# Performance work log

Hardware: AMD Instinct MI355X
Metric: run time of the kernel (lower is better)

The kernel has to match this reference:

```python
import jax, jax.numpy as jnp
import numpy as np

N_NODES = 100000
N_EDGES = 3200000
D_IN = 128
D_HID = 128
D_FF = 256
N_CLASSES = 26
N_GRAPHS = 512


def setup_inputs() -> dict:
    key = jax.random.key(0)
    ks = jax.random.split(key, 12)
    s = 0.05
    return {
        "x": jax.random.normal(ks[0], (N_NODES, D_IN), dtype=jnp.float32),
        "edge_index": jax.random.randint(ks[1], (2, N_EDGES), 0, N_NODES, dtype=jnp.int64),
        "batch": jnp.sort(jax.random.randint(ks[2], (N_NODES,), 0, N_GRAPHS, dtype=jnp.int64)),
        "W1": jax.random.normal(ks[3], (D_IN, D_HID), dtype=jnp.float32) * s,
        "b1": jnp.zeros((D_HID,), dtype=jnp.float32),
        "W2": jax.random.normal(ks[4], (D_HID, D_HID), dtype=jnp.float32) * s,
        "b2": jnp.zeros((D_HID,), dtype=jnp.float32),
        "W3": jax.random.normal(ks[5], (D_HID, D_HID), dtype=jnp.float32) * s,
        "b3": jnp.zeros((D_HID,), dtype=jnp.float32),
        "Wfc": jax.random.normal(ks[6], (D_HID, D_FF), dtype=jnp.float32) * s,
        "bfc": jnp.zeros((D_FF,), dtype=jnp.float32),
        "Wfc2": jax.random.normal(ks[7], (D_FF, N_CLASSES), dtype=jnp.float32) * s,
        "bfc2": jnp.zeros((N_CLASSES,), dtype=jnp.float32),
    }


def _gcn_layer(x, src, dst, norm, W, b):
    # GCNConv: h = x @ W; out[dst] += norm_e * h[src]; out += b
    h = x @ W                                   # [N, D]
    msg = h[src] * norm[:, None]                # [E+N, D] gather + scale
    agg = jax.ops.segment_sum(msg, dst, num_segments=N_NODES)
    return agg + b


def reference(x, edge_index, batch, W1, b1, W2, b2, W3, b3, Wfc, bfc, Wfc2, bfc2):
    # add self-loops (PyG GCNConv default) and compute symmetric normalization once
    loop = jnp.arange(N_NODES, dtype=edge_index.dtype)
    src = jnp.concatenate([edge_index[0], loop])
    dst = jnp.concatenate([edge_index[1], loop])
    deg = jax.ops.segment_sum(jnp.ones_like(dst, dtype=x.dtype), dst, num_segments=N_NODES)
    dinv = jnp.where(deg > 0, jax.lax.rsqrt(deg), 0.0)
    norm = dinv[src] * dinv[dst]               # D^{-1/2} A_hat D^{-1/2}

    h = jax.nn.relu(_gcn_layer(x, src, dst, norm, W1, b1))
    h = jax.nn.relu(_gcn_layer(h, src, dst, norm, W2, b2))
    h = jax.nn.relu(_gcn_layer(h, src, dst, norm, W3, b3))

    # global mean pool over graphs
    sums = jax.ops.segment_sum(h, batch, num_segments=N_GRAPHS)       # [G, D]
    cnts = jax.ops.segment_sum(jnp.ones((h.shape[0],), h.dtype), batch, num_segments=N_GRAPHS)
    pooled = sums / jnp.maximum(cnts, 1.0)[:, None]

    out = jax.nn.relu(pooled @ Wfc + bfc)       # dropout is identity at inference
    return out @ Wfc2 + bfc2                    # [G, num_classes]
```

## Files before the change

### kernel.cpp

```cpp
#include <hip/hip_runtime.h>
#include <hip/hip_bf16.h>

typedef __bf16 bf16;
typedef __attribute__((ext_vector_type(8))) __bf16 bf16x8;
typedef __attribute__((ext_vector_type(4))) float f32x4;

constexpr int N_NODES   = 100000;
constexpr int N_PAD     = 100032;
constexpr int D         = 128;
constexpr int D_FF      = 256;
constexpr int N_CLASSES = 26;
constexpr int N_GRAPHS  = 512;
constexpr int NB1       = 256;
constexpr int NBUCK     = (N_NODES + 511) / 512;

__device__ inline float2 bf2f(unsigned u) {
    float lo = __uint_as_float(u << 16);
    float hi = __uint_as_float(u & 0xffff0000u);
    return make_float2(lo, hi);
}

__device__ inline void nt_store_bf16(bf16* p, float f) {
    bf16 v = (bf16)f;
    short s = *reinterpret_cast<short*>(&v);
    __builtin_nontemporal_store(s, reinterpret_cast<short*>(p));
}


__global__ __launch_bounds__(1024) void p1_hist(const int* __restrict__ edst,
                                                int* __restrict__ gcount, int e) {
    __shared__ int cnt[NBUCK];
    for (int t = threadIdx.x; t < NBUCK; t += 1024) cnt[t] = 0;
    __syncthreads();
    int chunk = (e + NB1 - 1) / NB1;
    int lo = blockIdx.x * chunk;
    int hi = min(e, lo + chunk);
    for (int i = lo + threadIdx.x; i < hi; i += 1024)
        atomicAdd(&cnt[edst[i] >> 9], 1);
    __syncthreads();
    for (int t = threadIdx.x; t < NBUCK; t += 1024)
        gcount[t * NB1 + blockIdx.x] = cnt[t];
}

__global__ __launch_bounds__(256) void scan1(const int* __restrict__ in,
                                             int* out, int* bsum, int n) {
    __shared__ int sd[256];
    int i = blockIdx.x * 256 + threadIdx.x;
    int v = (i < n) ? in[i] : 0;
    sd[threadIdx.x] = v; __syncthreads();
    for (int off = 1; off < 256; off <<= 1) {
        int t = (threadIdx.x >= off) ? sd[threadIdx.x - off] : 0;
        __syncthreads();
        sd[threadIdx.x] += t;
        __syncthreads();
    }
    if (i < n) out[i] = sd[threadIdx.x] - v;
    if (threadIdx.x == 255) bsum[blockIdx.x] = sd[255];
}

__global__ __launch_bounds__(1024) void misc_kernel(const int* __restrict__ bsum,
                                                    int* __restrict__ boff, int nb,
                                                    const int* __restrict__ batch,
                                                    int* __restrict__ starts, int n,
                                                    const float* __restrict__ W0,
                                                    const float* __restrict__ W1,
                                                    const float* __restrict__ W2,
                                                    bf16* __restrict__ WT3,
                                                    float* __restrict__ gsum) {
    int t = threadIdx.x;
    if (blockIdx.x == 0) {
        if (t <= N_GRAPHS) {
            int lo = 0, hi = n;
            while (lo < hi) {
                int mid = (lo + hi) >> 1;
                if (batch[mid] < t) lo = mid + 1; else hi = mid;
            }
            starts[t] = lo;
        }
        __shared__ int sd[1024];
        int v = (t < nb) ? bsum[t] : 0;
        sd[t] = v; __syncthreads();
        for (int off = 1; off < 1024; off <<= 1) {
            int x = (t >= off) ? sd[t - off] : 0;
            __syncthreads();
            sd[t] += x;
            __syncthreads();
        }
        if (t < nb) boff[t] = sd[t] - v;
    } else if (blockIdx.x <= 48) {
        int idx = (blockIdx.x - 1) * 1024 + t;
        int l = idx >> 14;
        int rem = idx & 16383;
        int nn = rem >> 7;
        int kk = rem & 127;
        const float* W = (l == 0) ? W0 : (l == 1) ? W1 : W2;
        WT3[idx] = (bf16)W[kk * D + nn];
    } else {
        int idx = (blockIdx.x - 49) * 1024 + t;
        f32x4 z = {0.f, 0.f, 0.f, 0.f};
        *((f32x4*)gsum + idx) = z;
    }
}

__global__ __launch_bounds__(1024) void p3_scatter(const int* __restrict__ esrc,
                                                   const int* __restrict__ edst,
                                                   const int* __restrict__ gbase,
                                                   const int* __restrict__ boff,
                                                   int* __restrict__ ebuf, int e) {
    __shared__ int cur[NBUCK];
    for (int t = threadIdx.x; t < NBUCK; t += 1024)
        cur[t] = gbase[t * NB1 + blockIdx.x] + boff[t];
    __syncthreads();
    int chunk = (e + NB1 - 1) / NB1;
    int lo = blockIdx.x * chunk;
    int hi = min(e, lo + chunk);
    for (int i = lo + threadIdx.x; i < hi; i += 1024) {
        int d = edst[i], s = esrc[i];
        int pos = atomicAdd(&cur[d >> 9], 1);
        ebuf[pos] = (s << 9) | (d & 511);
    }
}

__global__ __launch_bounds__(1024) void p45_fill(const int* __restrict__ ebuf,
                                                 const int* __restrict__ gbase,
                                                 const int* __restrict__ boff,
                                                 float* __restrict__ dinv,
                                                 int* __restrict__ rowptr,
                                                 int* __restrict__ csrc, int e, int n) {
    __shared__ int cnt[512];
    __shared__ int ps[512];
    __shared__ int cur[512];
    int b = blockIdx.x, t = threadIdx.x;
    if (t < 512) cnt[t] = 0;
    __syncthreads();
    int lo = gbase[b * NB1] + boff[b];
    int hi = (b + 1 < NBUCK) ? gbase[(b + 1) * NB1] + boff[b + 1] : e;
    for (int i = lo + t; i < hi; i += 1024)
        atomicAdd(&cnt[ebuf[i] & 511], 1);
    __syncthreads();
    int a = (t < 512) ? cnt[t] : 0;
    if (t < 512) ps[t] = a;
    __syncthreads();
    for (int off = 1; off < 512; off <<= 1) {
        int v = (t >= off && t < 512) ? ps[t - off] : 0;
        __syncthreads();
        if (t < 512) ps[t] += v;
        __syncthreads();
    }
    if (t < 512) {
        int g0 = lo + ps[t] - a;
        int node = b * 512 + t;
        cur[t] = g0;
        if (node < n) {
            rowptr[node] = g0;
            dinv[node] = 1.0f / sqrtf((float)(a + 1));
        }
    }
    if (b == 0 && t == 0) rowptr[n] = e;
    __syncthreads();
    for (int i = lo + t; i < hi; i += 1024) {
        int pe = ebuf[i];
        int pos = atomicAdd(&cur[pe & 511], 1);
        csrc[pos] = pe >> 9;
    }
}


__global__ __launch_bounds__(256) void gemm_f32_kernel(const float* __restrict__ A,
                                                       const bf16* __restrict__ WT,
                                                       bf16* __restrict__ C,
                                                       const float* __restrict__ dinv, int n) {
    int wave = threadIdx.x >> 6;
    int lane = threadIdx.x & 63;
    int m16  = lane & 15;
    int quad = lane >> 4;
    int row0 = blockIdx.x * 64 + wave * 16;
    int arowi = row0 + m16;

    bf16x8 a[4];
    const float* arow = A + (size_t)arowi * D + quad * 8;
#pragma unroll
    for (int kt = 0; kt < 4; ++kt) {
        f32x4 f0 = {0.f, 0.f, 0.f, 0.f};
        f32x4 f1 = {0.f, 0.f, 0.f, 0.f};
        if (arowi < n) {
            f0 = __builtin_nontemporal_load((const f32x4*)(arow + kt * 32));
            f1 = __builtin_nontemporal_load((const f32x4*)(arow + kt * 32 + 4));
        }
        bf16x8 v = { (bf16)f0[0], (bf16)f0[1], (bf16)f0[2], (bf16)f0[3],
                     (bf16)f1[0], (bf16)f1[1], (bf16)f1[2], (bf16)f1[3] };
        a[kt] = v;
    }

    float sc[4];
#pragma unroll
    for (int r = 0; r < 4; ++r) {
        int rr = row0 + quad * 4 + r;
        sc[r] = (rr < n) ? dinv[rr] : 0.f;
    }

#pragma unroll
    for (int nt = 0; nt < 8; ++nt) {
        f32x4 acc = {0.f, 0.f, 0.f, 0.f};
        const bf16* brow = WT + (nt * 16 + m16) * D + quad * 8;
#pragma unroll
        for (int kt = 0; kt < 4; ++kt) {
            bf16x8 b = *(const bf16x8*)(brow + kt * 32);
            acc = __builtin_amdgcn_mfma_f32_16x16x32_bf16(a[kt], b, acc, 0, 0, 0);
        }
#pragma unroll
        for (int r = 0; r < 4; ++r)
            nt_store_bf16(&C[(row0 + quad * 4 + r) * D + nt * 16 + m16], sc[r] * acc[r]);
    }
}

__device__ inline void agg_node(const bf16* __restrict__ h, int v, int n, int c,
                                const int* __restrict__ rowptr,
                                const int* __restrict__ csrc,
                                const float* __restrict__ dinv,
                                float& dv, float acc[8]) {
    int s = 0, e = 0;
    dv = 0.f;
    if (v < n) { s = rowptr[v]; e = rowptr[v + 1]; dv = dinv[v]; }
#pragma unroll
    for (int d = 0; d < 8; ++d) acc[d] = 0.f;
    if (v < n) {
        uint4 u = *(const uint4*)(h + (size_t)v * D + c * 8);
        float2 f0 = bf2f(u.x), f1 = bf2f(u.y), f2 = bf2f(u.z), f3 = bf2f(u.w);
        acc[0] = f0.x; acc[1] = f0.y; acc[2] = f1.x; acc[3] = f1.y;
        acc[4] = f2.x; acc[5] = f2.y; acc[6] = f3.x; acc[7] = f3.y;
    }
    int j = s;
    for (; j + 3 < e; j += 4) {
        int s0 = __builtin_nontemporal_load(csrc + j);
        int s1 = __builtin_nontemporal_load(csrc + j + 1);
        int s2 = __builtin_nontemporal_load(csrc + j + 2);
        int s3 = __builtin_nontemporal_load(csrc + j + 3);
        uint4 u0 = *(const uint4*)(h + (size_t)s0 * D + c * 8);
        uint4 u1 = *(const uint4*)(h + (size_t)s1 * D + c * 8);
        uint4 u2 = *(const uint4*)(h + (size_t)s2 * D + c * 8);
        uint4 u3 = *(const uint4*)(h + (size_t)s3 * D + c * 8);
        {
            float2 a0 = bf2f(u0.x), a1 = bf2f(u0.y), a2 = bf2f(u0.z), a3 = bf2f(u0.w);
            acc[0] += a0.x; acc[1] += a0.y; acc[2] += a1.x; acc[3] += a1.y;
            acc[4] += a2.x; acc[5] += a2.y; acc[6] += a3.x; acc[7] += a3.y;
        }
        {
            float2 a0 = bf2f(u1.x), a1 = bf2f(u1.y), a2 = bf2f(u1.z), a3 = bf2f(u1.w);
            acc[0] += a0.x; acc[1] += a0.y; acc[2] += a1.x; acc[3] += a1.y;
            acc[4] += a2.x; acc[5] += a2.y; acc[6] += a3.x; acc[7] += a3.y;
        }
        {
            float2 a0 = bf2f(u2.x), a1 = bf2f(u2.y), a2 = bf2f(u2.z), a3 = bf2f(u2.w);
            acc[0] += a0.x; acc[1] += a0.y; acc[2] += a1.x; acc[3] += a1.y;
            acc[4] += a2.x; acc[5] += a2.y; acc[6] += a3.x; acc[7] += a3.y;
        }
        {
            float2 a0 = bf2f(u3.x), a1 = bf2f(u3.y), a2 = bf2f(u3.z), a3 = bf2f(u3.w);
            acc[0] += a0.x; acc[1] += a0.y; acc[2] += a1.x; acc[3] += a1.y;
            acc[4] += a2.x; acc[5] += a2.y; acc[6] += a3.x; acc[7] += a3.y;
        }
    }
    for (; j < e; ++j) {
        int s0 = __builtin_nontemporal_load(csrc + j);
        uint4 u0 = *(const uint4*)(h + (size_t)s0 * D + c * 8);
        float2 a0 = bf2f(u0.x), a1 = bf2f(u0.y), a2 = bf2f(u0.z), a3 = bf2f(u0.w);
        acc[0] += a0.x; acc[1] += a0.y; acc[2] += a1.x; acc[3] += a1.y;
        acc[4] += a2.x; acc[5] += a2.y; acc[6] += a3.x; acc[7] += a3.y;
    }
}

__global__ __launch_bounds__(256) void spmm_gemm_kernel(const bf16* __restrict__ h,
                                                        const int* __restrict__ rowptr,
                                                        const int* __restrict__ csrc,
                                                        const float* __restrict__ dinv,
                                                        const float* __restrict__ bias,
                                                        const bf16* __restrict__ WT,
                                                        bf16* __restrict__ C, int n) {
    __shared__ bf16 tile[16][136];
    int t = threadIdx.x;
    int grp = t >> 4;
    int c   = t & 15;
    int v   = blockIdx.x * 16 + grp;
    float dv, acc[8];
    agg_node(h, v, n, c, rowptr, csrc, dinv, dv, acc);
    {
        float4 bi0 = *(const float4*)(bias + c * 8);
        float4 bi1 = *(const float4*)(bias + c * 8 + 4);
        bf16x8 o;
        o[0] = (bf16)fmaxf(fmaf(dv, acc[0], bi0.x), 0.f);
        o[1] = (bf16)fmaxf(fmaf(dv, acc[1], bi0.y), 0.f);
        o[2] = (bf16)fmaxf(fmaf(dv, acc[2], bi0.z), 0.f);
        o[3] = (bf16)fmaxf(fmaf(dv, acc[3], bi0.w), 0.f);
        o[4] = (bf16)fmaxf(fmaf(dv, acc[4], bi1.x), 0.f);
        o[5] = (bf16)fmaxf(fmaf(dv, acc[5], bi1.y), 0.f);
        o[6] = (bf16)fmaxf(fmaf(dv, acc[6], bi1.z), 0.f);
        o[7] = (bf16)fmaxf(fmaf(dv, acc[7], bi1.w), 0.f);
        *(bf16x8*)(&tile[grp][c * 8]) = o;
    }
    __syncthreads();

    int wave = t >> 6, lane = t & 63;
    int m16 = lane & 15, quad = lane >> 4;
    bf16x8 a[4];
#pragma unroll
    for (int kt = 0; kt < 4; ++kt)
        a[kt] = *(const bf16x8*)(&tile[m16][quad * 8 + kt * 32]);

    int base = blockIdx.x * 16;
    float sc[4];
#pragma unroll
    for (int r = 0; r < 4; ++r) {
        int rr = base + quad * 4 + r;
        sc[r] = (rr < n) ? dinv[rr] : 0.f;
    }

#pragma unroll
    for (int nt2 = 0; nt2 < 2; ++nt2) {
        int nt = wave * 2 + nt2;
        f32x4 accq = {0.f, 0.f, 0.f, 0.f};
        const bf16* brow = WT + (nt * 16 + m16) * D + quad * 8;
#pragma unroll
        for (int kt = 0; kt < 4; ++kt) {
            bf16x8 b = *(const bf16x8*)(brow + kt * 32);
            accq = __builtin_amdgcn_mfma_f32_16x16x32_bf16(a[kt], b, accq, 0, 0, 0);
        }
#pragma unroll
        for (int r = 0; r < 4; ++r)
            nt_store_bf16(&C[(size_t)(base + quad * 4 + r) * D + nt * 16 + m16],
                          sc[r] * accq[r]);
    }
}

__global__ __launch_bounds__(256) void spmm2_pool_kernel(const bf16* __restrict__ h,
                                                         const int* __restrict__ rowptr,
                                                         const int* __restrict__ csrc,
                                                         const float* __restrict__ dinv,
                                                         const float* __restrict__ bias,
                                                         const int* __restrict__ batch,
                                                         float* __restrict__ gsum, int n) {
    __shared__ float tile[16][D];
    __shared__ int gid[16];
    int t = threadIdx.x;
    int grp = t >> 4;
    int c   = t & 15;
    int v   = blockIdx.x * 16 + grp;
    float dv, acc[8];
    agg_node(h, v, n, c, rowptr, csrc, dinv, dv, acc);
    float4 bi0 = *(const float4*)(bias + c * 8);
    float4 bi1 = *(const float4*)(bias + c * 8 + 4);
    float r0 = fmaxf(fmaf(dv, acc[0], bi0.x), 0.f);
    float r1 = fmaxf(fmaf(dv, acc[1], bi0.y), 0.f);
    float r2 = fmaxf(fmaf(dv, acc[2], bi0.z), 0.f);
    float r3 = fmaxf(fmaf(dv, acc[3], bi0.w), 0.f);
    float r4 = fmaxf(fmaf(dv, acc[4], bi1.x), 0.f);
    float r5 = fmaxf(fmaf(dv, acc[5], bi1.y), 0.f);
    float r6 = fmaxf(fmaf(dv, acc[6], bi1.z), 0.f);
    float r7 = fmaxf(fmaf(dv, acc[7], bi1.w), 0.f);
    if (v >= n) { r0 = r1 = r2 = r3 = r4 = r5 = r6 = r7 = 0.f; }
    tile[grp][c * 8 + 0] = r0; tile[grp][c * 8 + 1] = r1;
    tile[grp][c * 8 + 2] = r2; tile[grp][c * 8 + 3] = r3;
    tile[grp][c * 8 + 4] = r4; tile[grp][c * 8 + 5] = r5;
    tile[grp][c * 8 + 6] = r6; tile[grp][c * 8 + 7] = r7;
    if (c == 0) gid[grp] = (v < n) ? batch[v] : -1;
    __syncthreads();
    if (t < D) {
        int curg = gid[0];
        float sum = 0.f;
        if (curg >= 0) {
#pragma unroll 1
            for (int k = 0; k < 16; ++k) {
                int gg = gid[k];
                if (gg < 0) break;
                if (gg != curg) {
                    atomicAdd(&gsum[(size_t)curg * D + t], sum);
                    curg = gg; sum = 0.f;
                }
                sum += tile[k][t];
            }
            atomicAdd(&gsum[(size_t)curg * D + t], sum);
        }
    }
}

__global__ __launch_bounds__(256) void fc_head_kernel(const float* __restrict__ gsum,
                                                      const int* __restrict__ starts,
                                                      const float* __restrict__ Wfc,
                                                      const float* __restrict__ bfc,
                                                      const float* __restrict__ Wfc2,
                                                      const float* __restrict__ bfc2,
                                                      float* __restrict__ out) {
    __shared__ float pr[D];
    __shared__ float hid[D_FF];
    __shared__ float red[N_CLASSES][9];
    int g = blockIdx.x, t = threadIdx.x;
    if (t < D) {
        float ccount = fmaxf((float)(starts[g + 1] - starts[g]), 1.0f);
        pr[t] = gsum[(size_t)g * D + t] / ccount;
    }
    __syncthreads();
    float a0 = 0.f, a1 = 0.f, a2 = 0.f, a3 = 0.f;
    for (int k = 0; k < D; k += 4) {
        a0 = fmaf(pr[k],     Wfc[k * D_FF + t],       a0);
        a1 = fmaf(pr[k + 1], Wfc[(k + 1) * D_FF + t], a1);
        a2 = fmaf(pr[k + 2], Wfc[(k + 2) * D_FF + t], a2);
        a3 = fmaf(pr[k + 3], Wfc[(k + 3) * D_FF + t], a3);
    }
    hid[t] = fmaxf((a0 + a1) + (a2 + a3) + bfc[t], 0.f);
    __syncthreads();
    if (t < N_CLASSES * 8) {
        int cls = t >> 3, kk = t & 7;
        float o = 0.f;
        for (int k = kk; k < D_FF; k += 8)
            o = fmaf(hid[k], Wfc2[k * N_CLASSES + cls], o);
        red[cls][kk] = o;
    }
    __syncthreads();
    if (t < N_CLASSES) {
        float o = bfc2[t];
#pragma unroll
        for (int k = 0; k < 8; ++k) o += red[t][k];
        out[g * N_CLASSES + t] = o;
    }
}


extern "C" void kernel_launch(void* const* d_in, const int* in_sizes, int n_in,
                              void* d_out, int out_size, void* d_ws, size_t ws_size,
                              hipStream_t stream) {
    const float* x     = (const float*)d_in[0];
    const int*   eidx  = (const int*)d_in[1];
    const int*   batch = (const int*)d_in[2];
    const float* W[3]  = { (const float*)d_in[3], (const float*)d_in[5], (const float*)d_in[7] };
    const float* b[3]  = { (const float*)d_in[4], (const float*)d_in[6], (const float*)d_in[8] };
    const float* Wfc   = (const float*)d_in[9];
    const float* bfc   = (const float*)d_in[10];
    const float* Wfc2  = (const float*)d_in[11];
    const float* bfc2  = (const float*)d_in[12];
    float* out = (float*)d_out;

    const int E = in_sizes[1] / 2;
    const int N = in_sizes[0] / D;
    const int* esrc = eidx;
    const int* edst = eidx + E;

    uint8_t* base = (uint8_t*)d_ws;
    size_t off = 0;
    auto alloc = [&](size_t bytes) -> void* {
        void* p = base + off;
        off = (off + bytes + 255) & ~(size_t)255;
        return p;
    };
    bf16*  hA     = (bf16*) alloc((size_t)N_PAD * D * 2);
    bf16*  hB     = (bf16*) alloc((size_t)N_PAD * D * 2);
    bf16*  WT3    = (bf16*) alloc((size_t)3 * D * D * 2);
    int*   csrc   = (int*)  alloc((size_t)E * 4);
    int*   ebuf   = (int*)  alloc((size_t)E * 4);
    int*   gcount = (int*)  alloc((size_t)NBUCK * NB1 * 4);
    int*   gbase  = (int*)  alloc((size_t)(NBUCK * NB1 + 1) * 4);
    int*   rowptr = (int*)  alloc((size_t)(N + 1) * 4);
    float* dinv   = (float*)alloc((size_t)N * 4);
    int*   bsum   = (int*)  alloc(4096);
    int*   boff   = (int*)  alloc(4096);
    int*   starts = (int*)  alloc((size_t)(N_GRAPHS + 1) * 4);
    float* gsum   = (float*)alloc((size_t)N_GRAPHS * D * 4);
    (void)ws_size; (void)n_in; (void)out_size;

    const int GB  = N_PAD / 64;
    const int SGB = (N + 15) / 16;
    const int GCN = NBUCK * NB1;
    const int GCB = (GCN + 255) / 256;

    p1_hist<<<NB1, 1024, 0, stream>>>(edst, gcount, E);
    scan1<<<GCB, 256, 0, stream>>>(gcount, gbase, bsum, GCN);
    misc_kernel<<<65, 1024, 0, stream>>>(bsum, boff, GCB, batch, starts, N,
                                         W[0], W[1], W[2], WT3, gsum);
    p3_scatter<<<NB1, 1024, 0, stream>>>(esrc, edst, gbase, boff, ebuf, E);
    p45_fill<<<NBUCK, 1024, 0, stream>>>(ebuf, gbase, boff, dinv, rowptr, csrc, E, N);

    gemm_f32_kernel<<<GB, 256, 0, stream>>>(x, WT3, hA, dinv, N);
    spmm_gemm_kernel<<<SGB, 256, 0, stream>>>(hA, rowptr, csrc, dinv, b[0],
                                              WT3 + (size_t)1 * D * D, hB, N);
    spmm_gemm_kernel<<<SGB, 256, 0, stream>>>(hB, rowptr, csrc, dinv, b[1],
                                              WT3 + (size_t)2 * D * D, hA, N);
    spmm2_pool_kernel<<<SGB, 256, 0, stream>>>(hA, rowptr, csrc, dinv, b[2],
                                               batch, gsum, N);

    fc_head_kernel<<<N_GRAPHS, 256, 0, stream>>>(gsum, starts, Wfc, bfc, Wfc2, bfc2, out);
}
```

Measured before the change: 617.6 us.

## Fuse GCN layers and head into one cooperative persistent kernel with grid syncs

Replaces the separate GEMM, two SpMM+GEMM, SpMM+pool and FC-head launches with one cooperative persistent kernel that grid-strides over tiles and uses grid.sync between stages. The histogram and misc setup kernels are merged into one launch, and the block scan gets its own small kernel. Nontemporal loads and stores are also replaced with plain accesses. The aim is to cut launch overhead and inter-kernel gaps, at the cost of grid-wide barriers, persistent-loop overhead and occupancy limited to co-resident blocks.

After: 1.279 ms. +107.0%, slower.

```diff
diff --git a/kernel.cpp b/kernel.cpp
--- a/kernel.cpp
+++ b/kernel.cpp
@@ -1,5 +1,8 @@
 #include <hip/hip_runtime.h>
 #include <hip/hip_bf16.h>
+#include <hip/hip_cooperative_groups.h>
+
+namespace cg = cooperative_groups;
 
 typedef __bf16 bf16;
 typedef __attribute__((ext_vector_type(8))) __bf16 bf16x8;
@@ -13,6 +16,8 @@
 constexpr int N_GRAPHS  = 512;
 constexpr int NB1       = 256;
 constexpr int NBUCK     = (N_NODES + 511) / 512;
+constexpr int GB        = N_PAD / 64;
+constexpr int SGB       = N_NODES / 16;
 
 __device__ inline float2 bf2f(unsigned u) {
     float lo = __uint_as_float(u << 16);
@@ -20,26 +25,54 @@
     return make_float2(lo, hi);
 }
 
-__device__ inline void nt_store_bf16(bf16* p, float f) {
-    bf16 v = (bf16)f;
-    short s = *reinterpret_cast<short*>(&v);
-    __builtin_nontemporal_store(s, reinterpret_cast<short*>(p));
-}
-
-
-__global__ __launch_bounds__(1024) void p1_hist(const int* __restrict__ edst,
-                                                int* __restrict__ gcount, int e) {
-    __shared__ int cnt[NBUCK];
-    for (int t = threadIdx.x; t < NBUCK; t += 1024) cnt[t] = 0;
-    __syncthreads();
-    int chunk = (e + NB1 - 1) / NB1;
-    int lo = blockIdx.x * chunk;
-    int hi = min(e, lo + chunk);
-    for (int i = lo + threadIdx.x; i < hi; i += 1024)
-        atomicAdd(&cnt[edst[i] >> 9], 1);
-    __syncthreads();
-    for (int t = threadIdx.x; t < NBUCK; t += 1024)
-        gcount[t * NB1 + blockIdx.x] = cnt[t];
+
+__global__ __launch_bounds__(1024) void p1misc_kernel(const int* __restrict__ edst,
+                                                      int* __restrict__ gcount, int e,
+                                                      const int* __restrict__ batch,
+                                                      int* __restrict__ starts, int n,
+                                                      const float* __restrict__ W0,
+                                                      const float* __restrict__ W1,
+                                                      const float* __restrict__ W2,
+                                                      bf16* __restrict__ WT3,
+                                                      float* __restrict__ gsum) {
+    int t = threadIdx.x;
+    if (blockIdx.x < NB1) {
+        __shared__ int cnt[NBUCK];
+        for (int q = t; q < NBUCK; q += 1024) cnt[q] = 0;
+        __syncthreads();
+        int chunk = (e + NB1 - 1) / NB1;
+        int lo = blockIdx.x * chunk;
+        int hi = min(e, lo + chunk);
+        for (int i = lo + t; i < hi; i += 1024)
+            atomicAdd(&cnt[edst[i] >> 9], 1);
+        __syncthreads();
+        for (int q = t; q < NBUCK; q += 1024)
+            gcount[q * NB1 + blockIdx.x] = cnt[q];
+    } else {
+        int mb = blockIdx.x - NB1;
+        if (mb == 0) {
+            if (t <= N_GRAPHS) {
+                int lo = 0, hi = n;
+                while (lo < hi) {
+                    int mid = (lo + hi) >> 1;
+                    if (batch[mid] < t) lo = mid + 1; else hi = mid;
+                }
+                starts[t] = lo;
+            }
+        } else if (mb <= 48) {
+            int idx = (mb - 1) * 1024 + t;
+            int l = idx >> 14;
+            int rem = idx & 16383;
+            int nn = rem >> 7;
+            int kk = rem & 127;
+            const float* W = (l == 0) ? W0 : (l == 1) ? W1 : W2;
+            WT3[idx] = (bf16)W[kk * D + nn];
+        } else {
+            int idx = (mb - 49) * 1024 + t;
+            f32x4 z = {0.f, 0.f, 0.f, 0.f};
+            *((f32x4*)gsum + idx) = z;
+        }
+    }
 }
 
 __global__ __launch_bounds__(256) void scan1(const int* __restrict__ in,
@@ -58,48 +91,19 @@
     if (threadIdx.x == 255) bsum[blockIdx.x] = sd[255];
 }
 
-__global__ __launch_bounds__(1024) void misc_kernel(const int* __restrict__ bsum,
-                                                    int* __restrict__ boff, int nb,
-                                                    const int* __restrict__ batch,
-                                                    int* __restrict__ starts, int n,
-                                                    const float* __restrict__ W0,
-                                                    const float* __restrict__ W1,
-                                                    const float* __restrict__ W2,
-                                                    bf16* __restrict__ WT3,
-                                                    float* __restrict__ gsum) {
+__global__ __launch_bounds__(1024) void scan2k(const int* __restrict__ bsum,
+                                               int* __restrict__ boff, int nb) {
+    __shared__ int sd[1024];
     int t = threadIdx.x;
-    if (blockIdx.x == 0) {
-        if (t <= N_GRAPHS) {
-            int lo = 0, hi = n;
-            while (lo < hi) {
-                int mid = (lo + hi) >> 1;
-                if (batch[mid] < t) lo = mid + 1; else hi = mid;
-            }
-            starts[t] = lo;
-        }
-        __shared__ int sd[1024];
-        int v = (t < nb) ? bsum[t] : 0;
-        sd[t] = v; __syncthreads();
-        for (int off = 1; off < 1024; off <<= 1) {
-            int x = (t >= off) ? sd[t - off] : 0;
-            __syncthreads();
-            sd[t] += x;
-            __syncthreads();
-        }
-        if (t < nb) boff[t] = sd[t] - v;
-    } else if (blockIdx.x <= 48) {
-        int idx = (blockIdx.x - 1) * 1024 + t;
-        int l = idx >> 14;
-        int rem = idx & 16383;
-        int nn = rem >> 7;
-        int kk = rem & 127;
-        const float* W = (l == 0) ? W0 : (l == 1) ? W1 : W2;
-        WT3[idx] = (bf16)W[kk * D + nn];
-    } else {
-        int idx = (blockIdx.x - 49) * 1024 + t;
-        f32x4 z = {0.f, 0.f, 0.f, 0.f};
-        *((f32x4*)gsum + idx) = z;
-    }
+    int v = (t < nb) ? bsum[t] : 0;
+    sd[t] = v; __syncthreads();
+    for (int off = 1; off < 1024; off <<= 1) {
+        int x = (t >= off) ? sd[t - off] : 0;
+        __syncthreads();
+        sd[t] += x;
+        __syncthreads();
+    }
+    if (t < nb) boff[t] = sd[t] - v;
 }
 
 __global__ __launch_bounds__(1024) void p3_scatter(const int* __restrict__ esrc,
@@ -165,55 +169,6 @@
     }
 }
 
-
-__global__ __launch_bounds__(256) void gemm_f32_kernel(const float* __restrict__ A,
-                                                       const bf16* __restrict__ WT,
-                                                       bf16* __restrict__ C,
-                                                       const float* __restrict__ dinv, int n) {
-    int wave = threadIdx.x >> 6;
-    int lane = threadIdx.x & 63;
-    int m16  = lane & 15;
-    int quad = lane >> 4;
-    int row0 = blockIdx.x * 64 + wave * 16;
-    int arowi = row0 + m16;
-
-    bf16x8 a[4];
-    const float* arow = A + (size_t)arowi * D + quad * 8;
-#pragma unroll
-    for (int kt = 0; kt < 4; ++kt) {
-        f32x4 f0 = {0.f, 0.f, 0.f, 0.f};
-        f32x4 f1 = {0.f, 0.f, 0.f, 0.f};
-        if (arowi < n) {
-            f0 = __builtin_nontemporal_load((const f32x4*)(arow + kt * 32));
-            f1 = __builtin_nontemporal_load((const f32x4*)(arow + kt * 32 + 4));
-        }
-        bf16x8 v = { (bf16)f0[0], (bf16)f0[1], (bf16)f0[2], (bf16)f0[3],
-                     (bf16)f1[0], (bf16)f1[1], (bf16)f1[2], (bf16)f1[3] };
-        a[kt] = v;
-    }
-
-    float sc[4];
-#pragma unroll
-    for (int r = 0; r < 4; ++r) {
-        int rr = row0 + quad * 4 + r;
-        sc[r] = (rr < n) ? dinv[rr] : 0.f;
-    }
-
-#pragma unroll
-    for (int nt = 0; nt < 8; ++nt) {
-        f32x4 acc = {0.f, 0.f, 0.f, 0.f};
-        const bf16* brow = WT + (nt * 16 + m16) * D + quad * 8;
-#pragma unroll
-        for (int kt = 0; kt < 4; ++kt) {
-            bf16x8 b = *(const bf16x8*)(brow + kt * 32);
-            acc = __builtin_amdgcn_mfma_f32_16x16x32_bf16(a[kt], b, acc, 0, 0, 0);
-        }
-#pragma unroll
-        for (int r = 0; r < 4; ++r)
-            nt_store_bf16(&C[(row0 + quad * 4 + r) * D + nt * 16 + m16], sc[r] * acc[r]);
-    }
-}
-
 __device__ inline void agg_node(const bf16* __restrict__ h, int v, int n, int c,
                                 const int* __restrict__ rowptr,
                                 const int* __restrict__ csrc,
@@ -232,10 +187,7 @@
     }
     int j = s;
     for (; j + 3 < e; j += 4) {
-        int s0 = __builtin_nontemporal_load(csrc + j);
-        int s1 = __builtin_nontemporal_load(csrc + j + 1);
-        int s2 = __builtin_nontemporal_load(csrc + j + 2);
-        int s3 = __builtin_nontemporal_load(csrc + j + 3);
+        int s0 = csrc[j], s1 = csrc[j + 1], s2 = csrc[j + 2], s3 = csrc[j + 3];
         uint4 u0 = *(const uint4*)(h + (size_t)s0 * D + c * 8);
         uint4 u1 = *(const uint4*)(h + (size_t)s1 * D + c * 8);
         uint4 u2 = *(const uint4*)(h + (size_t)s2 * D + c * 8);
@@ -262,7 +214,7 @@
         }
     }
     for (; j < e; ++j) {
-        int s0 = __builtin_nontemporal_load(csrc + j);
+        int s0 = csrc[j];
         uint4 u0 = *(const uint4*)(h + (size_t)s0 * D + c * 8);
         float2 a0 = bf2f(u0.x), a1 = bf2f(u0.y), a2 = bf2f(u0.z), a3 = bf2f(u0.w);
         acc[0] += a0.x; acc[1] += a0.y; acc[2] += a1.x; acc[3] += a1.y;
@@ -270,23 +222,24 @@
     }
 }
 
-__global__ __launch_bounds__(256) void spmm_gemm_kernel(const bf16* __restrict__ h,
-                                                        const int* __restrict__ rowptr,
-                                                        const int* __restrict__ csrc,
-                                                        const float* __restrict__ dinv,
-                                                        const float* __restrict__ bias,
-                                                        const bf16* __restrict__ WT,
-                                                        bf16* __restrict__ C, int n) {
-    __shared__ bf16 tile[16][136];
+__device__ inline void agg_gemm_tiles(const bf16* __restrict__ h,
+                                      const int* __restrict__ rowptr,
+                                      const int* __restrict__ csrc,
+                                      const float* __restrict__ dinv,
+                                      const float* __restrict__ bias,
+                                      const bf16* __restrict__ WT,
+                                      bf16* __restrict__ C, int n,
+                                      bf16 (*tb)[136]) {
     int t = threadIdx.x;
-    int grp = t >> 4;
-    int c   = t & 15;
-    int v   = blockIdx.x * 16 + grp;
-    float dv, acc[8];
-    agg_node(h, v, n, c, rowptr, csrc, dinv, dv, acc);
-    {
-        float4 bi0 = *(const float4*)(bias + c * 8);
-        float4 bi1 = *(const float4*)(bias + c * 8 + 4);
+    int grp = t >> 4, c = t & 15;
+    int wave = t >> 6, lane = t & 63;
+    int m16 = lane & 15, quad = lane >> 4;
+    float4 bi0 = *(const float4*)(bias + c * 8);
+    float4 bi1 = *(const float4*)(bias + c * 8 + 4);
+    for (int tile = blockIdx.x; tile < SGB; tile += gridDim.x) {
+        int v = tile * 16 + grp;
+        float dv, acc[8];
+        agg_node(h, v, n, c, rowptr, csrc, dinv, dv, acc);
         bf16x8 o;
         o[0] = (bf16)fmaxf(fmaf(dv, acc[0], bi0.x), 0.f);
         o[1] = (bf16)fmaxf(fmaf(dv, acc[1], bi0.y), 0.f);
@@ -296,131 +249,179 @@
         o[5] = (bf16)fmaxf(fmaf(dv, acc[5], bi1.y), 0.f);
         o[6] = (bf16)fmaxf(fmaf(dv, acc[6], bi1.z), 0.f);
         o[7] = (bf16)fmaxf(fmaf(dv, acc[7], bi1.w), 0.f);
-        *(bf16x8*)(&tile[grp][c * 8]) = o;
-    }
-    __syncthreads();
-
-    int wave = t >> 6, lane = t & 63;
-    int m16 = lane & 15, quad = lane >> 4;
-    bf16x8 a[4];
-#pragma unroll
-    for (int kt = 0; kt < 4; ++kt)
-        a[kt] = *(const bf16x8*)(&tile[m16][quad * 8 + kt * 32]);
-
-    int base = blockIdx.x * 16;
-    float sc[4];
-#pragma unroll
-    for (int r = 0; r < 4; ++r) {
-        int rr = base + quad * 4 + r;
-        sc[r] = (rr < n) ? dinv[rr] : 0.f;
-    }
-
-#pragma unroll
-    for (int nt2 = 0; nt2 < 2; ++nt2) {
-        int nt = wave * 2 + nt2;
-        f32x4 accq = {0.f, 0.f, 0.f, 0.f};
-        const bf16* brow = WT + (nt * 16 + m16) * D + quad * 8;
-#pragma unroll
-        for (int kt = 0; kt < 4; ++kt) {
-            bf16x8 b = *(const bf16x8*)(brow + kt * 32);
-            accq = __builtin_amdgcn_mfma_f32_16x16x32_bf16(a[kt], b, accq, 0, 0, 0);
-        }
-#pragma unroll
-        for (int r = 0; r < 4; ++r)
-            nt_store_bf16(&C[(size_t)(base + quad * 4 + r) * D + nt * 16 + m16],
-                          sc[r] * accq[r]);
-    }
-}
-
-__global__ __launch_bounds__(256) void spmm2_pool_kernel(const bf16* __restrict__ h,
-                                                         const int* __restrict__ rowptr,
-                                                         const int* __restrict__ csrc,
-                                                         const float* __restrict__ dinv,
-                                                         const float* __restrict__ bias,
-                                                         const int* __restrict__ batch,
-                                                         float* __restrict__ gsum, int n) {
-    __shared__ float tile[16][D];
-    __shared__ int gid[16];
-    int t = threadIdx.x;
-    int grp = t >> 4;
-    int c   = t & 15;
-    int v   = blockIdx.x * 16 + grp;
-    float dv, acc[8];
-    agg_node(h, v, n, c, rowptr, csrc, dinv, dv, acc);
-    float4 bi0 = *(const float4*)(bias + c * 8);
-    float4 bi1 = *(const float4*)(bias + c * 8 + 4);
-    float r0 = fmaxf(fmaf(dv, acc[0], bi0.x), 0.f);
-    float r1 = fmaxf(fmaf(dv, acc[1], bi0.y), 0.f);
-    float r2 = fmaxf(fmaf(dv, acc[2], bi0.z), 0.f);
-    float r3 = fmaxf(fmaf(dv, acc[3], bi0.w), 0.f);
-    float r4 = fmaxf(fmaf(dv, acc[4], bi1.x), 0.f);
-    float r5 = fmaxf(fmaf(dv, acc[5], bi1.y), 0.f);
-    float r6 = fmaxf(fmaf(dv, acc[6], bi1.z), 0.f);
-    float r7 = fmaxf(fmaf(dv, acc[7], bi1.w), 0.f);
-    if (v >= n) { r0 = r1 = r2 = r3 = r4 = r5 = r6 = r7 = 0.f; }
-    tile[grp][c * 8 + 0] = r0; tile[grp][c * 8 + 1] = r1;
-    tile[grp][c * 8 + 2] = r2; tile[grp][c * 8 + 3] = r3;
-    tile[grp][c * 8 + 4] = r4; tile[grp][c * 8 + 5] = r5;
-    tile[grp][c * 8 + 6] = r6; tile[grp][c * 8 + 7] = r7;
-    if (c == 0) gid[grp] = (v < n) ? batch[v] : -1;
-    __syncthreads();
-    if (t < D) {
-        int curg = gid[0];
-        float sum = 0.f;
-        if (curg >= 0) {
-#pragma unroll 1
-            for (int k = 0; k < 16; ++k) {
-                int gg = gid[k];
-                if (gg < 0) break;
-                if (gg != curg) {
-                    atomicAdd(&gsum[(size_t)curg * D + t], sum);
-                    curg = gg; sum = 0.f;
-                }
-                sum += tile[k][t];
+        __syncthreads();
+        *(bf16x8*)(&tb[grp][c * 8]) = o;
+        __syncthreads();
+
+        bf16x8 a[4];
+#pragma unroll
+        for (int kt = 0; kt < 4; ++kt)
+            a[kt] = *(const bf16x8*)(&tb[m16][quad * 8 + kt * 32]);
+        int base = tile * 16;
+        float sc[4];
+#pragma unroll
+        for (int r = 0; r < 4; ++r) {
+            int rr = base + quad * 4 + r;
+            sc[r] = (rr < n) ? dinv[rr] : 0.f;
+        }
+#pragma unroll
+        for (int nt2 = 0; nt2 < 2; ++nt2) {
+            int nt = wave * 2 + nt2;
+            f32x4 q = {0.f, 0.f, 0.f, 0.f};
+            const bf16* brow = WT + (nt * 16 + m16) * D + quad * 8;
+#pragma unroll
+            for (int kt = 0; kt < 4; ++kt) {
+                bf16x8 bfr = *(const bf16x8*)(brow + kt * 32);
+                q = __builtin_amdgcn_mfma_f32_16x16x32_bf16(a[kt], bfr, q, 0, 0, 0);
             }
-            atomicAdd(&gsum[(size_t)curg * D + t], sum);
-        }
-    }
-}
-
-__global__ __launch_bounds__(256) void fc_head_kernel(const float* __restrict__ gsum,
-                                                      const int* __restrict__ starts,
-                                                      const float* __restrict__ Wfc,
-                                                      const float* __restrict__ bfc,
-                                                      const float* __restrict__ Wfc2,
-                                                      const float* __restrict__ bfc2,
-                                                      float* __restrict__ out) {
+#pragma unroll
+            for (int r = 0; r < 4; ++r)
+                C[(size_t)(base + quad * 4 + r) * D + nt * 16 + m16] = (bf16)(sc[r] * q[r]);
+        }
+    }
+}
+
+__global__ __launch_bounds__(256, 8) void mega_kernel(
+        const float* __restrict__ x, const bf16* __restrict__ WT3,
+        bf16* __restrict__ hA, bf16* __restrict__ hB,
+        const int* __restrict__ rowptr, const int* __restrict__ csrc,
+        const float* __restrict__ dinv,
+        const float* __restrict__ b0, const float* __restrict__ b1,
+        const float* __restrict__ b2,
+        const int* __restrict__ batch, float* __restrict__ gsum,
+        const int* __restrict__ starts,
+        const float* __restrict__ Wfc, const float* __restrict__ bfc,
+        const float* __restrict__ Wfc2, const float* __restrict__ bfc2,
+        float* __restrict__ out, int n) {
+    cg::grid_group grid = cg::this_grid();
+    __shared__ bf16  tb[16][136];
+    __shared__ float tf[16][D];
+    __shared__ int   gid[16];
     __shared__ float pr[D];
     __shared__ float hid[D_FF];
     __shared__ float red[N_CLASSES][9];
-    int g = blockIdx.x, t = threadIdx.x;
-    if (t < D) {
-        float ccount = fmaxf((float)(starts[g + 1] - starts[g]), 1.0f);
-        pr[t] = gsum[(size_t)g * D + t] / ccount;
-    }
-    __syncthreads();
-    float a0 = 0.f, a1 = 0.f, a2 = 0.f, a3 = 0.f;
-    for (int k = 0; k < D; k += 4) {
-        a0 = fmaf(pr[k],     Wfc[k * D_FF + t],       a0);
-        a1 = fmaf(pr[k + 1], Wfc[(k + 1) * D_FF + t], a1);
-        a2 = fmaf(pr[k + 2], Wfc[(k + 2) * D_FF + t], a2);
-        a3 = fmaf(pr[k + 3], Wfc[(k + 3) * D_FF + t], a3);
-    }
-    hid[t] = fmaxf((a0 + a1) + (a2 + a3) + bfc[t], 0.f);
-    __syncthreads();
-    if (t < N_CLASSES * 8) {
-        int cls = t >> 3, kk = t & 7;
-        float o = 0.f;
-        for (int k = kk; k < D_FF; k += 8)
-            o = fmaf(hid[k], Wfc2[k * N_CLASSES + cls], o);
-        red[cls][kk] = o;
-    }
-    __syncthreads();
-    if (t < N_CLASSES) {
-        float o = bfc2[t];
-#pragma unroll
-        for (int k = 0; k < 8; ++k) o += red[t][k];
-        out[g * N_CLASSES + t] = o;
+    int t = threadIdx.x;
+
+    {
+        int wave = t >> 6, lane = t & 63;
+        int m16 = lane & 15, quad = lane >> 4;
+        for (int tile = blockIdx.x; tile < GB; tile += gridDim.x) {
+            int row0 = tile * 64 + wave * 16;
+            int arowi = row0 + m16;
+            bf16x8 a[4];
+            const float* arow = x + (size_t)arowi * D + quad * 8;
+#pragma unroll
+            for (int kt = 0; kt < 4; ++kt) {
+                float4 f0 = make_float4(0.f, 0.f, 0.f, 0.f);
+                float4 f1 = make_float4(0.f, 0.f, 0.f, 0.f);
+                if (arowi < n) {
+                    f0 = *(const float4*)(arow + kt * 32);
+                    f1 = *(const float4*)(arow + kt * 32 + 4);
+                }
+                bf16x8 v = { (bf16)f0.x, (bf16)f0.y, (bf16)f0.z, (bf16)f0.w,
+                             (bf16)f1.x, (bf16)f1.y, (bf16)f1.z, (bf16)f1.w };
+                a[kt] = v;
+            }
+            float sc[4];
+#pragma unroll
+            for (int r = 0; r < 4; ++r) {
+                int rr = row0 + quad * 4 + r;
+                sc[r] = (rr < n) ? dinv[rr] : 0.f;
+            }
+#pragma unroll
+            for (int nt = 0; nt < 8; ++nt) {
+                f32x4 q = {0.f, 0.f, 0.f, 0.f};
+                const bf16* brow = WT3 + (nt * 16 + m16) * D + quad * 8;
+#pragma unroll
+                for (int kt = 0; kt < 4; ++kt) {
+                    bf16x8 bfr = *(const bf16x8*)(brow + kt * 32);
+                    q = __builtin_amdgcn_mfma_f32_16x16x32_bf16(a[kt], bfr, q, 0, 0, 0);
+                }
+#pragma unroll
+                for (int r = 0; r < 4; ++r)
+                    hA[(size_t)(row0 + quad * 4 + r) * D + nt * 16 + m16] = (bf16)(sc[r] * q[r]);
+            }
+        }
+    }
+    grid.sync();
+    agg_gemm_tiles(hA, rowptr, csrc, dinv, b0, WT3 + (size_t)1 * D * D, hB, n, tb);
+    grid.sync();
+    agg_gemm_tiles(hB, rowptr, csrc, dinv, b1, WT3 + (size_t)2 * D * D, hA, n, tb);
+    grid.sync();
+    {
+        int grp = t >> 4, c = t & 15;
+        float4 bi0 = *(const float4*)(b2 + c * 8);
+        float4 bi1 = *(const float4*)(b2 + c * 8 + 4);
+        for (int tile = blockIdx.x; tile < SGB; tile += gridDim.x) {
+            int v = tile * 16 + grp;
+            float dv, acc[8];
+            agg_node(hA, v, n, c, rowptr, csrc, dinv, dv, acc);
+            float r0 = fmaxf(fmaf(dv, acc[0], bi0.x), 0.f);
+            float r1 = fmaxf(fmaf(dv, acc[1], bi0.y), 0.f);
+            float r2 = fmaxf(fmaf(dv, acc[2], bi0.z), 0.f);
+            float r3 = fmaxf(fmaf(dv, acc[3], bi0.w), 0.f);
+            float r4 = fmaxf(fmaf(dv, acc[4], bi1.x), 0.f);
+            float r5 = fmaxf(fmaf(dv, acc[5], bi1.y), 0.f);
+            float r6 = fmaxf(fmaf(dv, acc[6], bi1.z), 0.f);
+            float r7 = fmaxf(fmaf(dv, acc[7], bi1.w), 0.f);
+            if (v >= n) { r0=r1=r2=r3=r4=r5=r6=r7 = 0.f; }
+            __syncthreads();
+            tf[grp][c * 8 + 0] = r0; tf[grp][c * 8 + 1] = r1;
+            tf[grp][c * 8 + 2] = r2; tf[grp][c * 8 + 3] = r3;
+            tf[grp][c * 8 + 4] = r4; tf[grp][c * 8 + 5] = r5;
+            tf[grp][c * 8 + 6] = r6; tf[grp][c * 8 + 7] = r7;
+            if (c == 0) gid[grp] = (v < n) ? batch[v] : -1;
+            __syncthreads();
+            if (t < D) {
+                int curg = gid[0];
+                float sum = 0.f;
+                if (curg >= 0) {
+#pragma unroll 1
+                    for (int k = 0; k < 16; ++k) {
+                        int gg = gid[k];
+                        if (gg < 0) break;
+                        if (gg != curg) {
+                            atomicAdd(&gsum[(size_t)curg * D + t], sum);
+                            curg = gg; sum = 0.f;
+                        }
+                        sum += tf[k][t];
+                    }
+                    atomicAdd(&gsum[(size_t)curg * D + t], sum);
+                }
+            }
+        }
+    }
+    grid.sync();
+    for (int g = blockIdx.x; g < N_GRAPHS; g += gridDim.x) {
+        __syncthreads();
+        if (t < D) {
+            float ccount = fmaxf((float)(starts[g + 1] - starts[g]), 1.0f);
+            pr[t] = gsum[(size_t)g * D + t] / ccount;
+        }
+        __syncthreads();
+        float a0 = 0.f, a1 = 0.f, a2 = 0.f, a3 = 0.f;
+        for (int k = 0; k < D; k += 4) {
+            a0 = fmaf(pr[k],     Wfc[k * D_FF + t],       a0);
+            a1 = fmaf(pr[k + 1], Wfc[(k + 1) * D_FF + t], a1);
+            a2 = fmaf(pr[k + 2], Wfc[(k + 2) * D_FF + t], a2);
+            a3 = fmaf(pr[k + 3], Wfc[(k + 3) * D_FF + t], a3);
+        }
+        hid[t] = fmaxf((a0 + a1) + (a2 + a3) + bfc[t], 0.f);
+        __syncthreads();
+        if (t < N_CLASSES * 8) {
+            int cls = t >> 3, kk = t & 7;
+            float o = 0.f;
+            for (int k = kk; k < D_FF; k += 8)
+                o = fmaf(hid[k], Wfc2[k * N_CLASSES + cls], o);
+            red[cls][kk] = o;
+        }
+        __syncthreads();
+        if (t < N_CLASSES) {
+            float o = bfc2[t];
+#pragma unroll
+            for (int k = 0; k < 8; ++k) o += red[t][k];
+            out[g * N_CLASSES + t] = o;
+        }
     }
 }
 
@@ -431,8 +432,12 @@
     const float* x     = (const float*)d_in[0];
     const int*   eidx  = (const int*)d_in[1];
     const int*   batch = (const int*)d_in[2];
-    const float* W[3]  = { (const float*)d_in[3], (const float*)d_in[5], (const float*)d_in[7] };
-    const float* b[3]  = { (const float*)d_in[4], (const float*)d_in[6], (const float*)d_in[8] };
+    const float* W0    = (const float*)d_in[3];
+    const float* b0    = (const float*)d_in[4];
+    const float* W1    = (const float*)d_in[5];
+    const float* b1    = (const float*)d_in[6];
+    const float* W2    = (const float*)d_in[7];
+    const float* b2    = (const float*)d_in[8];
     const float* Wfc   = (const float*)d_in[9];
     const float* bfc   = (const float*)d_in[10];
     const float* Wfc2  = (const float*)d_in[11];
@@ -466,25 +471,31 @@
     float* gsum   = (float*)alloc((size_t)N_GRAPHS * D * 4);
     (void)ws_size; (void)n_in; (void)out_size;
 
-    const int GB  = N_PAD / 64;
-    const int SGB = (N + 15) / 16;
     const int GCN = NBUCK * NB1;
     const int GCB = (GCN + 255) / 256;
 
-    p1_hist<<<NB1, 1024, 0, stream>>>(edst, gcount, E);
+    p1misc_kernel<<<NB1 + 65, 1024, 0, stream>>>(edst, gcount, E, batch, starts, N,
+                                                 W0, W1, W2, WT3, gsum);
     scan1<<<GCB, 256, 0, stream>>>(gcount, gbase, bsum, GCN);
-    misc_kernel<<<65, 1024, 0, stream>>>(bsum, boff, GCB, batch, starts, N,
-                                         W[0], W[1], W[2], WT3, gsum);
+    scan2k<<<1, 1024, 0, stream>>>(bsum, boff, GCB);
     p3_scatter<<<NB1, 1024, 0, stream>>>(esrc, edst, gbase, boff, ebuf, E);
     p45_fill<<<NBUCK, 1024, 0, stream>>>(ebuf, gbase, boff, dinv, rowptr, csrc, E, N);
 
-    gemm_f32_kernel<<<GB, 256, 0, stream>>>(x, WT3, hA, dinv, N);
-    spmm_gemm_kernel<<<SGB, 256, 0, stream>>>(hA, rowptr, csrc, dinv, b[0],
-                                              WT3 + (size_t)1 * D * D, hB, N);
-    spmm_gemm_kernel<<<SGB, 256, 0, stream>>>(hB, rowptr, csrc, dinv, b[1],
-                                              WT3 + (size_t)2 * D * D, hA, N);
-    spmm2_pool_kernel<<<SGB, 256, 0, stream>>>(hA, rowptr, csrc, dinv, b[2],
-                                               batch, gsum, N);
-
-    fc_head_kernel<<<N_GRAPHS, 256, 0, stream>>>(gsum, starts, Wfc, bfc, Wfc2, bfc2, out);
-}
+    static int s_nblk = 0;
+    if (s_nblk == 0) {
+        int mb = 0;
+        hipOccupancyMaxActiveBlocksPerMultiprocessor(&mb, mega_kernel, 256, 0);
+        if (mb < 1) mb = 1;
+        if (mb > 8) mb = 8;
+        s_nblk = mb * 256;
+    }
+    int nN = N;
+    void* margs[] = { (void*)&x, (void*)&WT3, (void*)&hA, (void*)&hB,
+                      (void*)&rowptr, (void*)&csrc, (void*)&dinv,
+                      (void*)&b0, (void*)&b1, (void*)&b2,
+                      (void*)&batch, (void*)&gsum, (void*)&starts,
+                      (void*)&Wfc, (void*)&bfc, (void*)&Wfc2, (void*)&bfc2,
+                      (void*)&out, (void*)&nN };
+    hipLaunchCooperativeKernel((const void*)mega_kernel, dim3(s_nblk), dim3(256),
+                               margs, 0, stream);
+}
```
